# Performance work log

Measured on AMD Instinct MI355X. Metric: run time of the kernel, lower is better.

The kernel has to match this reference:

```python
import jax, jax.numpy as jnp
import numpy as np
import math

N_DEC = 10
D = 128
H = 8
DFF = 4 * D
CODE_N = 127
PC_ROWS = 63
S = CODE_N + PC_ROWS
B = 512
EPS = 1e-5


def _ln(x, g, b):
    m = jnp.mean(x, axis=-1, keepdims=True)
    v = jnp.mean((x - m) ** 2, axis=-1, keepdims=True)
    return g * (x - m) / jnp.sqrt(v + EPS) + b


def _build_mask(pc_matrix):
    # True = blocked (masked_fill with -1e9), following get_mask in the source.
    A = (pc_matrix > 0)  # [m, n]
    Ai = A.astype(jnp.int32)
    vv = (Ai.T @ Ai) > 0  # var-var connectivity via shared checks
    eye_n = jnp.eye(CODE_N, dtype=bool)
    eye_m = jnp.eye(PC_ROWS, dtype=bool)
    top = jnp.concatenate([vv | eye_n, A.T], axis=1)          # [n, s]
    bot = jnp.concatenate([A, eye_m], axis=1)                  # [m, s]
    allow = jnp.concatenate([top, bot], axis=0)                # [s, s]
    return ~allow


def _mha(x, mask, Wq, bq, Wk, bk, Wv, bv, Wo, bo):
    b, s, d = x.shape
    dk = d // H
    q = (x @ Wq + bq).reshape(b, s, H, dk)
    k = (x @ Wk + bk).reshape(b, s, H, dk)
    v = (x @ Wv + bv).reshape(b, s, H, dk)
    scores = jnp.einsum('bqhd,bkhd->bhqk', q, k) / math.sqrt(dk)
    scores = jnp.where(mask[None, None], -1e9, scores)
    p = jax.nn.softmax(scores, axis=-1)
    o = jnp.einsum('bhqk,bkhd->bqhd', p, v).reshape(b, s, d)
    return o @ Wo + bo


def _forward(magnitude, syndrome, pc_matrix, src_embed,
             Wq, bq, Wk, bk, Wv, bv, Wo, bo,
             W1, b1, W2, b2,
             ln1_g, ln1_b, ln2_g, ln2_b,
             enc_g, enc_b, norm2_g, norm2_b,
             fin_w, fin_b, out_w, out_b):
    mask = _build_mask(pc_matrix)
    emb = jnp.concatenate([magnitude, syndrome], axis=-1)[..., None]  # [B, s, 1]
    x = src_embed[None] * emb  # [B, s, d]
    for i in range(N_DEC):
        # pre-norm attention sublayer
        h = _ln(x, ln1_g[i], ln1_b[i])
        x = x + _mha(h, mask, Wq[i], bq[i], Wk[i], bk[i], Wv[i], bv[i], Wo[i], bo[i])
        # pre-norm feed-forward sublayer (exact gelu like torch F.gelu default)
        h = _ln(x, ln2_g[i], ln2_b[i])
        ff = jax.nn.gelu(h @ W1[i] + b1[i], approximate=False) @ W2[i] + b2[i]
        x = x + ff
        if (i + 1) == N_DEC // 2 and N_DEC > 1:
            x = _ln(x, norm2_g, norm2_b)
    x = _ln(x, enc_g, enc_b)
    t = (x @ fin_w + fin_b)[..., 0]  # [B, s]
    return t @ out_w + out_b         # [B, n]


def setup_inputs() -> dict:
    key = jax.random.key(0)
    ks = jax.random.split(key, 32)
    sc = 0.02
    def nrm(k, shape, s=sc):
        return jax.random.normal(k, shape, dtype=jnp.float32) * s
    inp = {
        'magnitude': jax.random.normal(ks[0], (B, CODE_N), dtype=jnp.float32),
        'syndrome': jax.random.normal(ks[1], (B, PC_ROWS), dtype=jnp.float32),
        'pc_matrix': jax.random.randint(ks[2], (PC_ROWS, CODE_N), 0, 2, dtype=jnp.int32),
        'src_embed': nrm(ks[3], (S, D), 0.1),
        'Wq': nrm(ks[4], (N_DEC, D, D)), 'bq': jnp.zeros((N_DEC, D), jnp.float32),
        'Wk': nrm(ks[5], (N_DEC, D, D)), 'bk': jnp.zeros((N_DEC, D), jnp.float32),
        'Wv': nrm(ks[6], (N_DEC, D, D)), 'bv': jnp.zeros((N_DEC, D), jnp.float32),
        'Wo': nrm(ks[7], (N_DEC, D, D)), 'bo': jnp.zeros((N_DEC, D), jnp.float32),
        'W1': nrm(ks[8], (N_DEC, D, DFF)), 'b1': jnp.zeros((N_DEC, DFF), jnp.float32),
        'W2': nrm(ks[9], (N_DEC, DFF, D)), 'b2': jnp.zeros((N_DEC, D), jnp.float32),
        'ln1_g': jnp.ones((N_DEC, D), jnp.float32), 'ln1_b': jnp.zeros((N_DEC, D), jnp.float32),
        'ln2_g': jnp.ones((N_DEC, D), jnp.float32), 'ln2_b': jnp.zeros((N_DEC, D), jnp.float32),
        'enc_g': jnp.ones((D,), jnp.float32), 'enc_b': jnp.zeros((D,), jnp.float32),
        'norm2_g': jnp.ones((D,), jnp.float32), 'norm2_b': jnp.zeros((D,), jnp.float32),
        'fin_w': nrm(ks[10], (D, 1), 0.1), 'fin_b': jnp.zeros((1,), jnp.float32),
        'out_w': nrm(ks[11], (S, CODE_N), 0.1), 'out_b': jnp.zeros((CODE_N,), jnp.float32),
    }
    return inp


def reference(magnitude, syndrome, pc_matrix, src_embed,
              Wq, bq, Wk, bk, Wv, bv, Wo, bo,
              W1, b1, W2, b2,
              ln1_g, ln1_b, ln2_g, ln2_b,
              enc_g, enc_b, norm2_g, norm2_b,
              fin_w, fin_b, out_w, out_b):
    return _forward(magnitude, syndrome, pc_matrix, src_embed,
                    Wq, bq, Wk, bk, Wv, bv, Wo, bo,
                    W1, b1, W2, b2,
                    ln1_g, ln1_b, ln2_g, ln2_b,
                    enc_g, enc_b, norm2_g, norm2_b,
                    fin_w, fin_b, out_w, out_b)
```

## Files before the change

kernel.cpp:

```cpp
#include <hip/hip_runtime.h>
#include <math.h>

typedef unsigned int uint;
typedef unsigned short ushort;
typedef unsigned long long u64;

constexpr int B_    = 512;
constexpr int S_    = 190;
constexpr int D_    = 128;
constexpr int NDEC_ = 10;
constexpr int CN_   = 127;
constexpr int PCR_  = 63;
constexpr int MR_   = B_ * S_;

typedef __attribute__((ext_vector_type(4))) short bf16x4;
typedef __attribute__((ext_vector_type(8))) short bf16x8;
typedef __attribute__((ext_vector_type(4))) float f32x4;

__device__ __forceinline__ ushort f2b(float f) {
    uint x = __float_as_uint(f);
    uint r = x + 0x7fffu + ((x >> 16) & 1u);
    return (ushort)(r >> 16);
}
__device__ __forceinline__ float gelu_f(float v) {
    return 0.5f * v * (1.0f + erff(v * 0.70710678118654752f));
}
__device__ __forceinline__ int lds_e(int s, int c) { return s * 128 + (c ^ ((s & 7) << 3)); }

__device__ bool ablk(int i, int j, const u64* chk) {
    if (i < CN_ && j < CN_) return (i == j) || ((chk[i] & chk[j]) != 0ull);
    if (i < CN_)            return (chk[i] >> (j - CN_)) & 1ull;
    if (j < CN_)            return (chk[j] >> (i - CN_)) & 1ull;
    return i == j;
}
__global__ __launch_bounds__(256) void mbits2_k(const int* __restrict__ pc,
                                                uint* __restrict__ mb) {
    __shared__ u64 chk[CN_];
    int tid = threadIdx.x;
    if (tid < CN_) {
        u64 m = 0;
        for (int r = 0; r < PCR_; ++r)
            if (pc[r * CN_ + tid] > 0) m |= (1ull << r);
        chk[tid] = m;
    }
    __syncthreads();
    for (int idx = tid; idx < S_ * 8; idx += 256) {
        int i = idx >> 3, w = idx & 7;
        uint word = 0;
        if (w < 6)
            for (int b = 0; b < 32; ++b) {
                int j = w * 32 + b;
                if (j < S_ && ablk(i, j, chk)) word |= (1u << b);
            }
        mb[idx] = word;
    }
}

__global__ __launch_bounds__(256) void embln_k(const float* __restrict__ mag,
                                               const float* __restrict__ syn,
                                               const float* __restrict__ se,
                                               const float* __restrict__ g,
                                               const float* __restrict__ bta,
                                               float* __restrict__ x,
                                               ushort* __restrict__ h) {
    int wave = threadIdx.x >> 6;
    int lane = threadIdx.x & 63;
    long row = (long)blockIdx.x * 4 + wave;
    int b = (int)(row / S_), s = (int)(row % S_);
    float e = (s < CN_) ? mag[b * CN_ + s] : syn[b * PCR_ + (s - CN_)];
    float2 sev = *(const float2*)(se + s * D_ + lane * 2);
    float vx = sev.x * e, vy = sev.y * e;
    float sum = vx + vy, sq = vx * vx + vy * vy;
    #pragma unroll
    for (int o = 32; o; o >>= 1) { sum += __shfl_xor(sum, o); sq += __shfl_xor(sq, o); }
    float mean = sum * (1.0f / D_);
    float var  = sq * (1.0f / D_) - mean * mean;
    float inv  = rsqrtf(var + 1e-5f);
    float2 gv = *(const float2*)(g + lane * 2);
    float2 bv = *(const float2*)(bta + lane * 2);
    float o0 = gv.x * (vx - mean) * inv + bv.x;
    float o1 = gv.y * (vy - mean) * inv + bv.y;
    float2 xv; xv.x = vx; xv.y = vy;
    *(float2*)(x + row * D_ + lane * 2) = xv;
    uint packed = (uint)f2b(o0) | ((uint)f2b(o1) << 16);
    *(uint*)(h + row * D_ + lane * 2) = packed;
}

__global__ void wtr_k(const float* __restrict__ src, ushort* __restrict__ dst,
                      int K, int N) {
    int idx = blockIdx.x * 256 + threadIdx.x;
    int KN = K * N;
    int l = idx / KN, rem = idx % KN;
    int n = rem / K, k = rem % K;
    dst[idx] = f2b(src[(long)l * KN + (long)k * N + n]);
}
__global__ void wtr_qkv_k(const float* __restrict__ Wq, const float* __restrict__ Wk,
                          const float* __restrict__ Wv, ushort* __restrict__ dst) {
    int idx = blockIdx.x * 256 + threadIdx.x;
    int l = idx / (384 * 128);
    int rem = idx % (384 * 128);
    int n = rem >> 7, k = rem & 127;
    const float* src = (n < 128) ? Wq : (n < 256) ? Wk : Wv;
    dst[idx] = f2b(src[l * 16384 + k * 128 + (n & 127)]);
}
__global__ void bcat_k(const float* __restrict__ bq, const float* __restrict__ bk,
                       const float* __restrict__ bv, float* __restrict__ dst) {
    int idx = blockIdx.x * 256 + threadIdx.x;
    int l = idx / 384, n = idx % 384;
    const float* s = (n < 128) ? bq : (n < 256) ? bk : bv;
    dst[idx] = s[l * 128 + (n & 127)];
}

__global__ __launch_bounds__(256) void ln_k(const float* __restrict__ in,
                                            const float* __restrict__ g,
                                            const float* __restrict__ bta,
                                            ushort* __restrict__ outp) {
    int wave = threadIdx.x >> 6;
    int lane = threadIdx.x & 63;
    long row = (long)blockIdx.x * 4 + wave;
    const float* r = in + row * D_;
    float2 v = *(const float2*)(r + lane * 2);
    float sum = v.x + v.y;
    float sq  = v.x * v.x + v.y * v.y;
    #pragma unroll
    for (int o = 32; o; o >>= 1) { sum += __shfl_xor(sum, o); sq += __shfl_xor(sq, o); }
    float mean = sum * (1.0f / D_);
    float var  = sq * (1.0f / D_) - mean * mean;
    float inv  = rsqrtf(var + 1e-5f);
    float2 gv = *(const float2*)(g + lane * 2);
    float2 bv = *(const float2*)(bta + lane * 2);
    float o0 = gv.x * (v.x - mean) * inv + bv.x;
    float o1 = gv.y * (v.y - mean) * inv + bv.y;
    uint packed = (uint)f2b(o0) | ((uint)f2b(o1) << 16);
    *(uint*)(outp + row * D_ + lane * 2) = packed;
}

template <bool GELU>
__global__ __launch_bounds__(256) void gemm_k4(const ushort* __restrict__ A,
                                               const ushort* __restrict__ Wt,
                                               const float* __restrict__ bias,
                                               ushort* __restrict__ outp,
                                               int Nstride) {
    __shared__ ushort Al[128 * 128];
    __shared__ ushort Bl[128 * 128];
    const int tid = threadIdx.x;
    const int lane = tid & 63, wid = tid >> 6;
    const int lr = lane & 15, lh = lane >> 4;
    const long row0 = (long)blockIdx.x * 128;
    const int cb = blockIdx.y;
    const ushort* Wtb = Wt + cb * 128 * 128;

    #pragma unroll
    for (int i = 0; i < 8; ++i) {
        int idx = i * 256 + tid;
        int r = idx >> 4, s = idx & 15;
        uint4 d = *(const uint4*)(A + (row0 + r) * 128 + s * 8);
        *(uint4*)&Al[lds_e(r, s * 8)] = d;
        uint4 e = *(const uint4*)(Wtb + r * 128 + s * 8);
        *(uint4*)&Bl[lds_e(r, s * 8)] = e;
    }
    __syncthreads();

    f32x4 acc[2][8];
    #pragma unroll
    for (int i = 0; i < 2; ++i)
        #pragma unroll
        for (int j = 0; j < 8; ++j) { f32x4 z = {0.f,0.f,0.f,0.f}; acc[i][j] = z; }

    #pragma unroll
    for (int ks = 0; ks < 4; ++ks) {
        bf16x8 af[2], bfr[8];
        #pragma unroll
        for (int fi = 0; fi < 2; ++fi)
            af[fi] = *(const bf16x8*)&Al[lds_e((wid << 5) + (fi << 4) + lr, (ks << 5) + (lh << 3))];
        #pragma unroll
        for (int fj = 0; fj < 8; ++fj)
            bfr[fj] = *(const bf16x8*)&Bl[lds_e((fj << 4) + lr, (ks << 5) + (lh << 3))];
        #pragma unroll
        for (int fi = 0; fi < 2; ++fi)
            #pragma unroll
            for (int fj = 0; fj < 8; ++fj)
                acc[fi][fj] = __builtin_amdgcn_mfma_f32_16x16x32_bf16(af[fi], bfr[fj], acc[fi][fj], 0, 0, 0);
    }

    float bv[8];
    #pragma unroll
    for (int fj = 0; fj < 8; ++fj) bv[fj] = bias[cb * 128 + (fj << 4) + lr];
    #pragma unroll
    for (int fi = 0; fi < 2; ++fi)
        #pragma unroll
        for (int fj = 0; fj < 8; ++fj)
            #pragma unroll
            for (int rg = 0; rg < 4; ++rg) {
                long row = row0 + (wid << 5) + (fi << 4) + (lh << 2) + rg;
                float val = acc[fi][fj][rg] + bv[fj];
                if (GELU) val = gelu_f(val);
                outp[row * Nstride + cb * 128 + (fj << 4) + lr] = f2b(val);
            }
}

template <int LNMODE>
__global__ __launch_bounds__(256) void gemm_k3(const ushort* __restrict__ A,
                                               const ushort* __restrict__ Wt,
                                               const float* __restrict__ bias,
                                               const float* __restrict__ res,
                                               float* __restrict__ xout,
                                               ushort* __restrict__ hout,
                                               const float* __restrict__ lng,
                                               const float* __restrict__ lnb,
                                               int K) {
    __shared__ ushort Al[128 * 128];
    __shared__ ushort Bl[128 * 128];
    const int tid = threadIdx.x;
    const int lane = tid & 63, wid = tid >> 6;
    const int lr = lane & 15, lh = lane >> 4;
    const long row0 = (long)blockIdx.x * 128;

    f32x4 acc[2][8];
    #pragma unroll
    for (int i = 0; i < 2; ++i)
        #pragma unroll
        for (int j = 0; j < 8; ++j) { f32x4 z = {0.f, 0.f, 0.f, 0.f}; acc[i][j] = z; }

    for (int k0 = 0; k0 < K; k0 += 128) {
        #pragma unroll
        for (int i = 0; i < 8; ++i) {
            int idx = i * 256 + tid;
            int r = idx >> 4, s = idx & 15;
            uint4 d = *(const uint4*)(A + (row0 + r) * (long)K + k0 + s * 8);
            *(uint4*)&Al[lds_e(r, s * 8)] = d;
            uint4 e = *(const uint4*)(Wt + r * (long)K + k0 + s * 8);
            *(uint4*)&Bl[lds_e(r, s * 8)] = e;
        }
        __syncthreads();
        #pragma unroll
        for (int ks = 0; ks < 4; ++ks) {
            bf16x8 af[2], bfr[8];
            #pragma unroll
            for (int fi = 0; fi < 2; ++fi)
                af[fi] = *(const bf16x8*)&Al[lds_e((wid << 5) + (fi << 4) + lr, (ks << 5) + (lh << 3))];
            #pragma unroll
            for (int fj = 0; fj < 8; ++fj)
                bfr[fj] = *(const bf16x8*)&Bl[lds_e((fj << 4) + lr, (ks << 5) + (lh << 3))];
            #pragma unroll
            for (int fi = 0; fi < 2; ++fi)
                #pragma unroll
                for (int fj = 0; fj < 8; ++fj)
                    acc[fi][fj] = __builtin_amdgcn_mfma_f32_16x16x32_bf16(af[fi], bfr[fj], acc[fi][fj], 0, 0, 0);
        }
        __syncthreads();
    }

    #pragma unroll
    for (int fi = 0; fi < 2; ++fi) {
        #pragma unroll
        for (int rg = 0; rg < 4; ++rg) {
            long row = row0 + (wid << 5) + (fi << 4) + (lh << 2) + rg;
            float v[8], s1 = 0.f, s2 = 0.f;
            #pragma unroll
            for (int fj = 0; fj < 8; ++fj) {
                int col = (fj << 4) + lr;
                float val = acc[fi][fj][rg] + bias[col] + res[row * 128 + col];
                v[fj] = val; s1 += val; s2 += val * val;
            }
            if (LNMODE == 0) {
                #pragma unroll
                for (int fj = 0; fj < 8; ++fj)
                    xout[row * 128 + ((fj << 4) + lr)] = v[fj];
            } else {
                #pragma unroll
                for (int o = 1; o < 16; o <<= 1) {
                    s1 += __shfl_xor(s1, o);
                    s2 += __shfl_xor(s2, o);
                }
                float mean = s1 * (1.0f / 128.0f);
                float var  = s2 * (1.0f / 128.0f) - mean * mean;
                float inv  = rsqrtf(var + 1e-5f);
                #pragma unroll
                for (int fj = 0; fj < 8; ++fj) {
                    int col = (fj << 4) + lr;
                    float ln = lng[col] * (v[fj] - mean) * inv + lnb[col];
                    if (LNMODE == 1) {
                        xout[row * 128 + col] = v[fj];
                        hout[row * 128 + col] = f2b(ln);
                    } else {
                        xout[row * 128 + col] = ln;
                    }
                }
            }
        }
    }
}

__global__ __launch_bounds__(512) void attn4_k(const ushort* __restrict__ qkv,
                                               const uint* __restrict__ mb,
                                               const ushort* __restrict__ Wot,
                                               const float* __restrict__ bo,
                                               const float* __restrict__ lng,
                                               const float* __restrict__ lnb,
                                               float* __restrict__ x,
                                               ushort* __restrict__ hbuf) {
    __shared__ ushort ks[192 * 128];
    __shared__ ushort vs[192 * 128];
    const int b = blockIdx.x, tid = threadIdx.x;
    const long base = (long)b * S_ * 384;

    for (int idx = tid; idx < S_ * 16; idx += 512) {
        int r = idx >> 4, sl = idx & 15;
        uint4 uk = *(const uint4*)(qkv + base + (long)r * 384 + 128 + sl * 8);
        uint4 uv = *(const uint4*)(qkv + base + (long)r * 384 + 256 + sl * 8);
        int w = lds_e(r, sl * 8);
        *(uint4*)&ks[w] = uk;
        *(uint4*)&vs[w] = uv;
    }
    __syncthreads();

    const int h = tid >> 6;
    const int lane = tid & 63;
    const int lr = lane & 15, lh = lane >> 4;
    const int lh2 = lh & 1;

    bf16x8 kf[12];
    #pragma unroll
    for (int jt = 0; jt < 12; ++jt) {
        int j = jt * 16 + lr; if (j > 189) j = 189;
        bf16x8 v8 = *(const bf16x8*)&ks[lds_e(j, h * 16 + lh2 * 8)];
        if (lh >= 2) { bf16x8 z = {0,0,0,0,0,0,0,0}; v8 = z; }
        kf[jt] = v8;
    }
    bf16x4 vf[12];
    #pragma unroll
    for (int jt = 0; jt < 12; ++jt) {
        int j0 = jt * 16 + lh * 4;
        int c = h * 16 + lr;
        int ja = j0 + 0 > 189 ? 189 : j0 + 0;
        int jb = j0 + 1 > 189 ? 189 : j0 + 1;
        int jc = j0 + 2 > 189 ? 189 : j0 + 2;
        int jd = j0 + 3 > 189 ? 189 : j0 + 3;
        bf16x4 v4;
        v4[0] = (short)vs[lds_e(ja, c)];
        v4[1] = (short)vs[lds_e(jb, c)];
        v4[2] = (short)vs[lds_e(jc, c)];
        v4[3] = (short)vs[lds_e(jd, c)];
        vf[jt] = v4;
    }
    __syncthreads();

    #pragma unroll
    for (int i = 0; i < 4; ++i) {
        int idx = i * 512 + tid;
        int r = idx >> 4, sl = idx & 15;
        uint4 d = *(const uint4*)(Wot + r * 128 + sl * 8);
        *(uint4*)&vs[lds_e(r, sl * 8)] = d;
    }

    bf16x8 qf = *(const bf16x8*)(qkv + base + (long)lr * 384 + h * 16 + lh2 * 8);

    for (int qt = 0; qt < 12; ++qt) {
        f32x4 T[12];
        f32x4 zero = {0.f, 0.f, 0.f, 0.f};
        #pragma unroll
        for (int jt = 0; jt < 12; ++jt)
            T[jt] = __builtin_amdgcn_mfma_f32_16x16x32_bf16(kf[jt], qf, zero, 0, 0, 0);
        {
            int sn = (qt + 1) * 16 + lr; if (sn > 189) sn = 189;
            qf = *(const bf16x8*)(qkv + base + (long)sn * 384 + h * 16 + lh2 * 8);
        }
        int qc = qt * 16 + lr; if (qc > 189) qc = 189;
        uint mw[6];
        #pragma unroll
        for (int w = 0; w < 6; ++w) mw[w] = mb[qc * 8 + w];

        float p[12][4];
        float lsum = 0.f;
        #pragma unroll
        for (int jt = 0; jt < 12; ++jt) {
            uint word = mw[jt >> 1];
            #pragma unroll
            for (int r = 0; r < 4; ++r) {
                int bit = ((jt & 1) << 4) + 4 * lh + r;
                float e = __expf(T[jt][r] * 0.25f);
                float pv = ((word >> bit) & 1u) ? e : 0.f;
                p[jt][r] = pv;
                lsum += pv;
            }
        }
        lsum += __shfl_xor(lsum, 16);
        lsum += __shfl_xor(lsum, 32);
        float inv = 1.0f / lsum;

        f32x4 acc = {0.f, 0.f, 0.f, 0.f};
        #pragma unroll
        for (int jt = 0; jt < 12; ++jt) {
            uint lo, hi;
            float a0 = p[jt][0] * inv, a1 = p[jt][1] * inv;
            float a2 = p[jt][2] * inv, a3 = p[jt][3] * inv;
            asm("v_cvt_pk_bf16_f32 %0, %1, %2" : "=v"(lo) : "v"(a0), "v"(a1));
            asm("v_cvt_pk_bf16_f32 %0, %1, %2" : "=v"(hi) : "v"(a2), "v"(a3));
            uint2 u; u.x = lo; u.y = hi;
            bf16x4 pf = *(bf16x4*)&u;
            asm("s_nop 1\n\tv_mfma_f32_16x16x16_bf16 %0, %1, %2, %0"
                : "+v"(acc) : "v"(pf), "v"(vf[jt]));
        }
        asm volatile("s_nop 7\n\ts_nop 7" : "+v"(acc));

        #pragma unroll
        for (int r = 0; r < 4; ++r) {
            int qg = qt * 16 + 4 * lh + r;
            ks[lds_e(qg, h * 16 + lr)] = f2b(acc[r]);
        }
    }
    __syncthreads();

    if (h < 6) {
        const int w = h;
        f32x4 acc[2][8];
        #pragma unroll
        for (int i = 0; i < 2; ++i)
            #pragma unroll
            for (int j = 0; j < 8; ++j) { f32x4 z = {0.f,0.f,0.f,0.f}; acc[i][j] = z; }
        #pragma unroll
        for (int ksi = 0; ksi < 4; ++ksi) {
            bf16x8 af[2], bfr[8];
            #pragma unroll
            for (int fi = 0; fi < 2; ++fi)
                af[fi] = *(const bf16x8*)&ks[lds_e((w << 5) + (fi << 4) + lr, (ksi << 5) + (lh << 3))];
            #pragma unroll
            for (int fj = 0; fj < 8; ++fj)
                bfr[fj] = *(const bf16x8*)&vs[lds_e((fj << 4) + lr, (ksi << 5) + (lh << 3))];
            #pragma unroll
            for (int fi = 0; fi < 2; ++fi)
                #pragma unroll
                for (int fj = 0; fj < 8; ++fj)
                    acc[fi][fj] = __builtin_amdgcn_mfma_f32_16x16x32_bf16(af[fi], bfr[fj], acc[fi][fj], 0, 0, 0);
        }
        float bv[8], gv[8], bb[8];
        #pragma unroll
        for (int fj = 0; fj < 8; ++fj) {
            int col = (fj << 4) + lr;
            bv[fj] = bo[col]; gv[fj] = lng[col]; bb[fj] = lnb[col];
        }
        #pragma unroll
        for (int fi = 0; fi < 2; ++fi)
            #pragma unroll
            for (int rg = 0; rg < 4; ++rg) {
                int row = (w << 5) + (fi << 4) + (lh << 2) + rg;
                int rc = row > 189 ? 189 : row;
                long grow = (long)b * S_ + rc;
                float v[8], s1 = 0.f, s2 = 0.f;
                #pragma unroll
                for (int fj = 0; fj < 8; ++fj) {
                    int col = (fj << 4) + lr;
                    float val = acc[fi][fj][rg] + bv[fj] + x[grow * 128 + col];
                    v[fj] = val; s1 += val; s2 += val * val;
                }
                #pragma unroll
                for (int o = 1; o < 16; o <<= 1) {
                    s1 += __shfl_xor(s1, o);
                    s2 += __shfl_xor(s2, o);
                }
                float mean = s1 * (1.0f / 128.0f);
                float var  = s2 * (1.0f / 128.0f) - mean * mean;
                float inv  = rsqrtf(var + 1e-5f);
                if (row < S_) {
                    #pragma unroll
                    for (int fj = 0; fj < 8; ++fj) {
                        int col = (fj << 4) + lr;
                        x[grow * 128 + col] = v[fj];
                        hbuf[grow * 128 + col] = f2b(gv[fj] * (v[fj] - mean) * inv + bb[fj]);
                    }
                }
            }
    }
}

__global__ __launch_bounds__(256) void fin_k(const float* __restrict__ x,
                                             const float* __restrict__ g,
                                             const float* __restrict__ bta,
                                             const float* __restrict__ fw,
                                             const float* __restrict__ fb,
                                             float* __restrict__ t) {
    int wave = threadIdx.x >> 6;
    int lane = threadIdx.x & 63;
    long row = (long)blockIdx.x * 4 + wave;
    const float* r = x + row * D_;
    float2 v = *(const float2*)(r + lane * 2);
    float sum = v.x + v.y;
    float sq  = v.x * v.x + v.y * v.y;
    #pragma unroll
    for (int o = 32; o; o >>= 1) { sum += __shfl_xor(sum, o); sq += __shfl_xor(sq, o); }
    float mean = sum * (1.0f / D_);
    float var  = sq * (1.0f / D_) - mean * mean;
    float inv  = rsqrtf(var + 1e-5f);
    float2 gv = *(const float2*)(g + lane * 2);
    float2 bv = *(const float2*)(bta + lane * 2);
    float y0 = gv.x * (v.x - mean) * inv + bv.x;
    float y1 = gv.y * (v.y - mean) * inv + bv.y;
    float part = y0 * fw[lane * 2] + y1 * fw[lane * 2 + 1];
    #pragma unroll
    for (int o = 32; o; o >>= 1) part += __shfl_xor(part, o);
    if (lane == 0) t[row] = part + fb[0];
}

__global__ __launch_bounds__(128) void outgemm_k(const float* __restrict__ t,
                                                 const float* __restrict__ ow,
                                                 const float* __restrict__ ob,
                                                 float* __restrict__ out) {
    __shared__ float ts[S_];
    int b = blockIdx.x, tid = threadIdx.x;
    for (int i = tid; i < S_; i += 128) ts[i] = t[(long)b * S_ + i];
    __syncthreads();
    if (tid < CN_) {
        float acc = ob[tid];
        for (int s = 0; s < S_; ++s) acc = fmaf(ts[s], ow[s * CN_ + tid], acc);
        out[(long)b * CN_ + tid] = acc;
    }
}

extern "C" void kernel_launch(void* const* d_in, const int* in_sizes, int n_in,
                              void* d_out, int out_size, void* d_ws, size_t ws_size,
                              hipStream_t stream) {
    const float* mag  = (const float*)d_in[0];
    const float* syn  = (const float*)d_in[1];
    const int*   pc   = (const int*)  d_in[2];
    const float* se   = (const float*)d_in[3];
    const float* Wq   = (const float*)d_in[4];
    const float* bq   = (const float*)d_in[5];
    const float* Wk   = (const float*)d_in[6];
    const float* bk   = (const float*)d_in[7];
    const float* Wv   = (const float*)d_in[8];
    const float* bv   = (const float*)d_in[9];
    const float* Wo   = (const float*)d_in[10];
    const float* bo   = (const float*)d_in[11];
    const float* W1   = (const float*)d_in[12];
    const float* b1   = (const float*)d_in[13];
    const float* W2   = (const float*)d_in[14];
    const float* b2   = (const float*)d_in[15];
    const float* ln1g = (const float*)d_in[16];
    const float* ln1b = (const float*)d_in[17];
    const float* ln2g = (const float*)d_in[18];
    const float* ln2b = (const float*)d_in[19];
    const float* encg = (const float*)d_in[20];
    const float* encb = (const float*)d_in[21];
    const float* n2g  = (const float*)d_in[22];
    const float* n2b  = (const float*)d_in[23];
    const float* finw = (const float*)d_in[24];
    const float* finb = (const float*)d_in[25];
    const float* outw = (const float*)d_in[26];
    const float* outb = (const float*)d_in[27];
    float* out = (float*)d_out;

    char* p = (char*)d_ws;
    float*  x     = (float*) p;
    ushort* h     = (ushort*)(p + 49807360);
    ushort* qkv   = (ushort*)(p + 74711040);
    ushort* Wqkvt = (ushort*)(p + 174325760);
    ushort* Wot   = (ushort*)(p + 175308800);
    ushort* W1t   = (ushort*)(p + 175636480);
    ushort* W2t   = (ushort*)(p + 176947200);
    float*  bqkv  = (float*) (p + 178257920);
    uint*   mb    = (uint*)  (p + 178273280);
    float*  t     = (float*) (p + 178279360);
    ushort* ff1   = qkv;

    mbits2_k<<<1, 256, 0, stream>>>(pc, mb);
    wtr_qkv_k<<<1920, 256, 0, stream>>>(Wq, Wk, Wv, Wqkvt);
    wtr_k<<<640, 256, 0, stream>>>(Wo, Wot, 128, 128);
    wtr_k<<<2560, 256, 0, stream>>>(W1, W1t, 128, 512);
    wtr_k<<<2560, 256, 0, stream>>>(W2, W2t, 512, 128);
    bcat_k<<<15, 256, 0, stream>>>(bq, bk, bv, bqkv);
    embln_k<<<MR_ / 4, 256, 0, stream>>>(mag, syn, se, ln1g, ln1b, x, h);

    for (int i = 0; i < NDEC_; ++i) {
        gemm_k4<false><<<dim3(760, 3), 256, 0, stream>>>(
            h, Wqkvt + (long)i * 49152, bqkv + i * 384, qkv, 384);
        attn4_k<<<B_, 512, 0, stream>>>(
            qkv, mb, Wot + (long)i * 16384, bo + i * 128,
            ln2g + i * 128, ln2b + i * 128, x, h);
        gemm_k4<true><<<dim3(760, 4), 256, 0, stream>>>(
            h, W1t + (long)i * 65536, b1 + i * 512, ff1, 512);
        if (i == 4) {
            gemm_k3<2><<<760, 256, 0, stream>>>(
                ff1, W2t + (long)i * 65536, b2 + i * 128, x, x, nullptr,
                n2g, n2b, 512);
            ln_k<<<MR_ / 4, 256, 0, stream>>>(x, ln1g + 5 * 128, ln1b + 5 * 128, h);
        } else if (i == NDEC_ - 1) {
            gemm_k3<0><<<760, 256, 0, stream>>>(
                ff1, W2t + (long)i * 65536, b2 + i * 128, x, x, nullptr,
                nullptr, nullptr, 512);
        } else {
            gemm_k3<1><<<760, 256, 0, stream>>>(
                ff1, W2t + (long)i * 65536, b2 + i * 128, x, x, h,
                ln1g + (i + 1) * 128, ln1b + (i + 1) * 128, 512);
        }
    }

    fin_k<<<MR_ / 4, 256, 0, stream>>>(x, encg, encb, finw, finb, t);
    outgemm_k<<<B_, 128, 0, stream>>>(t, outw, outb, out);
}
```

Baseline: 2.147 ms.

## Split attention query tiles across two waves per head with 1024-thread blocks

Doubles the attention block to 1024 threads so each head gets two waves, each handling half of the 12 query tiles, and the output projection is spread over 12 waves with one 16-row tile each instead of 6 waves with two. This raises wave-level parallelism per block and shortens the serial per-wave query loop. In exchange each wave still loads the full K/V fragments (duplicated register loading), and the 1024-thread block with about 96KB of LDS may limit register budget per thread and occupancy.

```diff
diff --git a/kernel.cpp b/kernel.cpp
--- a/kernel.cpp
+++ b/kernel.cpp
@@ -292,20 +292,20 @@
     }
 }
 
-__global__ __launch_bounds__(512) void attn4_k(const ushort* __restrict__ qkv,
-                                               const uint* __restrict__ mb,
-                                               const ushort* __restrict__ Wot,
-                                               const float* __restrict__ bo,
-                                               const float* __restrict__ lng,
-                                               const float* __restrict__ lnb,
-                                               float* __restrict__ x,
-                                               ushort* __restrict__ hbuf) {
+__global__ __launch_bounds__(1024) void attn4_k(const ushort* __restrict__ qkv,
+                                                const uint* __restrict__ mb,
+                                                const ushort* __restrict__ Wot,
+                                                const float* __restrict__ bo,
+                                                const float* __restrict__ lng,
+                                                const float* __restrict__ lnb,
+                                                float* __restrict__ x,
+                                                ushort* __restrict__ hbuf) {
     __shared__ ushort ks[192 * 128];
     __shared__ ushort vs[192 * 128];
     const int b = blockIdx.x, tid = threadIdx.x;
     const long base = (long)b * S_ * 384;
 
-    for (int idx = tid; idx < S_ * 16; idx += 512) {
+    for (int idx = tid; idx < S_ * 16; idx += 1024) {
         int r = idx >> 4, sl = idx & 15;
         uint4 uk = *(const uint4*)(qkv + base + (long)r * 384 + 128 + sl * 8);
         uint4 uv = *(const uint4*)(qkv + base + (long)r * 384 + 256 + sl * 8);
@@ -315,7 +315,9 @@
     }
     __syncthreads();
 
-    const int h = tid >> 6;
+    const int wid = tid >> 6;
+    const int h = wid >> 1;
+    const int qh = wid & 1;
     const int lane = tid & 63;
     const int lr = lane & 15, lh = lane >> 4;
     const int lh2 = lh & 1;
@@ -346,93 +348,87 @@
     }
     __syncthreads();
 
-    #pragma unroll
-    for (int i = 0; i < 4; ++i) {
-        int idx = i * 512 + tid;
+    for (int idx = tid; idx < 128 * 16; idx += 1024) {
         int r = idx >> 4, sl = idx & 15;
         uint4 d = *(const uint4*)(Wot + r * 128 + sl * 8);
         *(uint4*)&vs[lds_e(r, sl * 8)] = d;
     }
 
-    bf16x8 qf = *(const bf16x8*)(qkv + base + (long)lr * 384 + h * 16 + lh2 * 8);
-
-    for (int qt = 0; qt < 12; ++qt) {
-        f32x4 T[12];
-        f32x4 zero = {0.f, 0.f, 0.f, 0.f};
-        #pragma unroll
-        for (int jt = 0; jt < 12; ++jt)
-            T[jt] = __builtin_amdgcn_mfma_f32_16x16x32_bf16(kf[jt], qf, zero, 0, 0, 0);
-        {
-            int sn = (qt + 1) * 16 + lr; if (sn > 189) sn = 189;
-            qf = *(const bf16x8*)(qkv + base + (long)sn * 384 + h * 16 + lh2 * 8);
-        }
-        int qc = qt * 16 + lr; if (qc > 189) qc = 189;
-        uint mw[6];
-        #pragma unroll
-        for (int w = 0; w < 6; ++w) mw[w] = mb[qc * 8 + w];
-
-        float p[12][4];
-        float lsum = 0.f;
-        #pragma unroll
-        for (int jt = 0; jt < 12; ++jt) {
-            uint word = mw[jt >> 1];
+    const int qt0 = qh * 6;
+    {
+        int sq = qt0 * 16 + lr;
+        bf16x8 qf = *(const bf16x8*)(qkv + base + (long)sq * 384 + h * 16 + lh2 * 8);
+
+        for (int qt = qt0; qt < qt0 + 6; ++qt) {
+            f32x4 T[12];
+            f32x4 zero = {0.f, 0.f, 0.f, 0.f};
+            #pragma unroll
+            for (int jt = 0; jt < 12; ++jt)
+                T[jt] = __builtin_amdgcn_mfma_f32_16x16x32_bf16(kf[jt], qf, zero, 0, 0, 0);
+            {
+                int sn = (qt + 1) * 16 + lr; if (sn > 189) sn = 189;
+                qf = *(const bf16x8*)(qkv + base + (long)sn * 384 + h * 16 + lh2 * 8);
+            }
+            int qc = qt * 16 + lr; if (qc > 189) qc = 189;
+            uint mw[6];
+            #pragma unroll
+            for (int w = 0; w < 6; ++w) mw[w] = mb[qc * 8 + w];
+
+            float p[12][4];
+            float lsum = 0.f;
+            #pragma unroll
+            for (int jt = 0; jt < 12; ++jt) {
+                uint word = mw[jt >> 1];
+                #pragma unroll
+                for (int r = 0; r < 4; ++r) {
+                    int bit = ((jt & 1) << 4) + 4 * lh + r;
+                    float e = __expf(T[jt][r] * 0.25f);
+                    float pv = ((word >> bit) & 1u) ? e : 0.f;
+                    p[jt][r] = pv;
+                    lsum += pv;
+                }
+            }
+            lsum += __shfl_xor(lsum, 16);
+            lsum += __shfl_xor(lsum, 32);
+            float inv = 1.0f / lsum;
+
+            f32x4 acc = {0.f, 0.f, 0.f, 0.f};
+            #pragma unroll
+            for (int jt = 0; jt < 12; ++jt) {
+                uint lo, hi;
+                float a0 = p[jt][0] * inv, a1 = p[jt][1] * inv;
+                float a2 = p[jt][2] * inv, a3 = p[jt][3] * inv;
+                asm("v_cvt_pk_bf16_f32 %0, %1, %2" : "=v"(lo) : "v"(a0), "v"(a1));
+                asm("v_cvt_pk_bf16_f32 %0, %1, %2" : "=v"(hi) : "v"(a2), "v"(a3));
+                uint2 u; u.x = lo; u.y = hi;
+                bf16x4 pf = *(bf16x4*)&u;
+                asm("s_nop 1\n\tv_mfma_f32_16x16x16_bf16 %0, %1, %2, %0"
+                    : "+v"(acc) : "v"(pf), "v"(vf[jt]));
+            }
+            asm volatile("s_nop 7\n\ts_nop 7" : "+v"(acc));
+
             #pragma unroll
             for (int r = 0; r < 4; ++r) {
-                int bit = ((jt & 1) << 4) + 4 * lh + r;
-                float e = __expf(T[jt][r] * 0.25f);
-                float pv = ((word >> bit) & 1u) ? e : 0.f;
-                p[jt][r] = pv;
-                lsum += pv;
-            }
-        }
-        lsum += __shfl_xor(lsum, 16);
-        lsum += __shfl_xor(lsum, 32);
-        float inv = 1.0f / lsum;
-
-        f32x4 acc = {0.f, 0.f, 0.f, 0.f};
-        #pragma unroll
-        for (int jt = 0; jt < 12; ++jt) {
-            uint lo, hi;
-            float a0 = p[jt][0] * inv, a1 = p[jt][1] * inv;
-            float a2 = p[jt][2] * inv, a3 = p[jt][3] * inv;
-            asm("v_cvt_pk_bf16_f32 %0, %1, %2" : "=v"(lo) : "v"(a0), "v"(a1));
-            asm("v_cvt_pk_bf16_f32 %0, %1, %2" : "=v"(hi) : "v"(a2), "v"(a3));
-            uint2 u; u.x = lo; u.y = hi;
-            bf16x4 pf = *(bf16x4*)&u;
-            asm("s_nop 1\n\tv_mfma_f32_16x16x16_bf16 %0, %1, %2, %0"
-                : "+v"(acc) : "v"(pf), "v"(vf[jt]));
-        }
-        asm volatile("s_nop 7\n\ts_nop 7" : "+v"(acc));
-
-        #pragma unroll
-        for (int r = 0; r < 4; ++r) {
-            int qg = qt * 16 + 4 * lh + r;
-            ks[lds_e(qg, h * 16 + lr)] = f2b(acc[r]);
+                int qg = qt * 16 + 4 * lh + r;
+                ks[lds_e(qg, h * 16 + lr)] = f2b(acc[r]);
+            }
         }
     }
     __syncthreads();
 
-    if (h < 6) {
-        const int w = h;
-        f32x4 acc[2][8];
-        #pragma unroll
-        for (int i = 0; i < 2; ++i)
-            #pragma unroll
-            for (int j = 0; j < 8; ++j) { f32x4 z = {0.f,0.f,0.f,0.f}; acc[i][j] = z; }
+    if (wid < 12) {
+        const int r0 = wid << 4;
+        f32x4 acc[8];
+        #pragma unroll
+        for (int j = 0; j < 8; ++j) { f32x4 z = {0.f,0.f,0.f,0.f}; acc[j] = z; }
         #pragma unroll
         for (int ksi = 0; ksi < 4; ++ksi) {
-            bf16x8 af[2], bfr[8];
-            #pragma unroll
-            for (int fi = 0; fi < 2; ++fi)
-                af[fi] = *(const bf16x8*)&ks[lds_e((w << 5) + (fi << 4) + lr, (ksi << 5) + (lh << 3))];
-            #pragma unroll
-            for (int fj = 0; fj < 8; ++fj)
-                bfr[fj] = *(const bf16x8*)&vs[lds_e((fj << 4) + lr, (ksi << 5) + (lh << 3))];
-            #pragma unroll
-            for (int fi = 0; fi < 2; ++fi)
-                #pragma unroll
-                for (int fj = 0; fj < 8; ++fj)
-                    acc[fi][fj] = __builtin_amdgcn_mfma_f32_16x16x32_bf16(af[fi], bfr[fj], acc[fi][fj], 0, 0, 0);
+            bf16x8 af = *(const bf16x8*)&ks[lds_e(r0 + lr, (ksi << 5) + (lh << 3))];
+            #pragma unroll
+            for (int fj = 0; fj < 8; ++fj) {
+                bf16x8 bfr = *(const bf16x8*)&vs[lds_e((fj << 4) + lr, (ksi << 5) + (lh << 3))];
+                acc[fj] = __builtin_amdgcn_mfma_f32_16x16x32_bf16(af, bfr, acc[fj], 0, 0, 0);
+            }
         }
         float bv[8], gv[8], bb[8];
         #pragma unroll
@@ -441,36 +437,34 @@
             bv[fj] = bo[col]; gv[fj] = lng[col]; bb[fj] = lnb[col];
         }
         #pragma unroll
-        for (int fi = 0; fi < 2; ++fi)
-            #pragma unroll
-            for (int rg = 0; rg < 4; ++rg) {
-                int row = (w << 5) + (fi << 4) + (lh << 2) + rg;
-                int rc = row > 189 ? 189 : row;
-                long grow = (long)b * S_ + rc;
-                float v[8], s1 = 0.f, s2 = 0.f;
+        for (int rg = 0; rg < 4; ++rg) {
+            int row = r0 + (lh << 2) + rg;
+            int rc = row > 189 ? 189 : row;
+            long grow = (long)b * S_ + rc;
+            float v[8], s1 = 0.f, s2 = 0.f;
+            #pragma unroll
+            for (int fj = 0; fj < 8; ++fj) {
+                int col = (fj << 4) + lr;
+                float val = acc[fj][rg] + bv[fj] + x[grow * 128 + col];
+                v[fj] = val; s1 += val; s2 += val * val;
+            }
+            #pragma unroll
+            for (int o = 1; o < 16; o <<= 1) {
+                s1 += __shfl_xor(s1, o);
+                s2 += __shfl_xor(s2, o);
+            }
+            float mean = s1 * (1.0f / 128.0f);
+            float var  = s2 * (1.0f / 128.0f) - mean * mean;
+            float inv  = rsqrtf(var + 1e-5f);
+            if (row < S_) {
                 #pragma unroll
                 for (int fj = 0; fj < 8; ++fj) {
                     int col = (fj << 4) + lr;
-                    float val = acc[fi][fj][rg] + bv[fj] + x[grow * 128 + col];
-                    v[fj] = val; s1 += val; s2 += val * val;
+                    x[grow * 128 + col] = v[fj];
+                    hbuf[grow * 128 + col] = f2b(gv[fj] * (v[fj] - mean) * inv + bb[fj]);
                 }
-                #pragma unroll
-                for (int o = 1; o < 16; o <<= 1) {
-                    s1 += __shfl_xor(s1, o);
-                    s2 += __shfl_xor(s2, o);
-                }
-                float mean = s1 * (1.0f / 128.0f);
-                float var  = s2 * (1.0f / 128.0f) - mean * mean;
-                float inv  = rsqrtf(var + 1e-5f);
-                if (row < S_) {
-                    #pragma unroll
-                    for (int fj = 0; fj < 8; ++fj) {
-                        int col = (fj << 4) + lr;
-                        x[grow * 128 + col] = v[fj];
-                        hbuf[grow * 128 + col] = f2b(gv[fj] * (v[fj] - mean) * inv + bb[fj]);
-                    }
-                }
-            }
+            }
+        }
     }
 }
 
@@ -574,7 +568,7 @@
     for (int i = 0; i < NDEC_; ++i) {
         gemm_k4<false><<<dim3(760, 3), 256, 0, stream>>>(
             h, Wqkvt + (long)i * 49152, bqkv + i * 384, qkv, 384);
-        attn4_k<<<B_, 512, 0, stream>>>(
+        attn4_k<<<B_, 1024, 0, stream>>>(
             qkv, mb, Wot + (long)i * 16384, bo + i * 128,
             ln2g + i * 128, ln2b + i * 128, x, h);
         gemm_k4<true><<<dim3(760, 4), 256, 0, stream>>>(
```

New measurement: 2.496 ms. 16.2% more time.
